# Kernel tuning notes

Hardware: AMD Instinct MI355X
Metric: run time of the kernel (lower is better)

The kernel has to match this reference:

```python
import jax, jax.numpy as jnp
import numpy as np

B, C, N, K, COUT = 8, 128, 10000, 16, 256


def setup_inputs() -> dict:
    key = jax.random.key(0)
    ks = jax.random.split(key, 8)
    x = jax.random.normal(ks[0], (B, C, N, 1), dtype=jnp.float32)
    edge_index = jax.random.randint(ks[1], (2, B, N, K), 0, N)
    s1 = 1.0 / np.sqrt(C)
    W1 = jax.random.uniform(ks[2], (C, C), jnp.float32, -s1, s1)   # nn1 1x1 conv weight
    b1 = jax.random.uniform(ks[3], (C,), jnp.float32, -s1, s1)
    Wp = jax.random.uniform(ks[4], (C, C), jnp.float32, -s1, s1)   # nn_pooling Linear
    bp = jax.random.uniform(ks[5], (C,), jnp.float32, -s1, s1)
    s2 = 1.0 / np.sqrt(2 * C)
    W2 = jax.random.uniform(ks[6], (COUT, 2 * C), jnp.float32, -s2, s2)  # nn2 1x1 conv
    b2 = jax.random.uniform(ks[7], (COUT,), jnp.float32, -s2, s2)
    return dict(x=x, edge_index=edge_index, W1=W1, b1=b1, Wp=Wp, bp=bp, W2=W2, b2=b2)


def reference(x, edge_index, W1, b1, Wp, bp, W2, b2):
    b, c, n, _ = x.shape
    k = edge_index.shape[-1]
    # nn1: 1x1 conv (channel mix) + ReLU -> [B,C,N,1]
    h = jax.nn.relu(jnp.einsum('bcns,dc->bdns', x, W1) + b1[None, :, None, None])
    # batched_index_select: gather neighbor features along vertex dim -> [B,C,N,K]
    hn = h[:, :, :, 0]                              # [B,C,N]
    idx = edge_index[0].reshape(b, 1, n * k)        # broadcast over C
    xj = jnp.take_along_axis(hn, idx, axis=2).reshape(b, c, n, k)
    # nn_pooling: Linear over channel dim + ReLU (transpose(1,3) in torch == act on C)
    xj = jax.nn.relu(jnp.einsum('bcnk,dc->bdnk', xj, Wp) + bp[None, :, None, None])
    # max-pool over neighbors, keepdim -> [B,C,N,1]
    xj = jnp.max(xj, axis=-1, keepdims=True)
    # concat along channels, nn2: 1x1 conv + ReLU -> [B,COUT,N,1]
    cat = jnp.concatenate([h, xj], axis=1)
    out = jax.nn.relu(jnp.einsum('bcns,dc->bdns', cat, W2) + b2[None, :, None, None])
    return out
```

## Files before the change

### kernel.cpp

```cpp
#include <hip/hip_runtime.h>

#define NODES 10000
#define BATCH 8
#define CH    128
#define KNB   16
#define CO    256

typedef __bf16 bf16x8 __attribute__((ext_vector_type(8)));
typedef float  f32x4  __attribute__((ext_vector_type(4)));

__device__ __forceinline__ unsigned short f2bf(float f) {
  unsigned u = __float_as_uint(f);
  u = (u + 0x7FFFu + ((u >> 16) & 1u)) >> 16;
  return (unsigned short)u;
}

__device__ __forceinline__ unsigned pkmax(unsigned a, unsigned b) {
  unsigned d;
  asm("v_pk_max_u16 %0, %1, %2" : "=v"(d) : "v"(a), "v"(b));
  return d;
}

__device__ __forceinline__ bf16x8 asbf8(uint4 u) {
  union { uint4 u; bf16x8 b; } c; c.u = u; return c.b;
}

__global__ __launch_bounds__(256) void prep(
    const float* __restrict__ W1, const float* __restrict__ Wp,
    const float* __restrict__ W2,
    unsigned short* __restrict__ W1b, unsigned short* __restrict__ Wpb,
    unsigned short* __restrict__ W2b)
{
  int i = blockIdx.x * 256 + threadIdx.x;
  const float* src; unsigned short* dst; int off;
  if (i < 4096)      { src = W1; dst = W1b; off = i; }
  else if (i < 8192) { src = Wp; dst = Wpb; off = i - 4096; }
  else               { src = W2; dst = W2b; off = i - 8192; }
  float4 v = ((const float4*)src)[off];
  ushort4 o;
  o.x = f2bf(v.x); o.y = f2bf(v.y); o.z = f2bf(v.z); o.w = f2bf(v.w);
  ((ushort4*)dst)[off] = o;
}

template<int MODE>
__global__ __launch_bounds__(256) void gemm_node(
    const unsigned short* __restrict__ Wb, const float* __restrict__ bias,
    const void* __restrict__ In, unsigned short* __restrict__ Out)
{
  const int b  = blockIdx.y;
  const int n0 = blockIdx.x * 64;
  const int t  = threadIdx.x;
  const int lane = t & 63, w = t >> 6;
  const int lm = lane & 15, q = lane >> 4;

  __shared__ unsigned short Bt[64 * 128];
  char* BtB = (char*)Bt;

  if (MODE == 0) {
    const float* X = (const float*)In + (size_t)b * CH * NODES;
#pragma unroll
    for (int rep = 0; rep < 4; ++rep) {
      int flat = t + rep * 256;
      int c2 = flat >> 4, n4 = flat & 15;
      int c  = c2 * 2;
      int gn = n0 + n4 * 4;
      float4 a0 = make_float4(0.f,0.f,0.f,0.f), a1 = a0;
      if (gn < NODES) {
        a0 = *(const float4*)(X + (size_t)c * NODES + gn);
        a1 = *(const float4*)(X + (size_t)(c + 1) * NODES + gn);
      }
      float v0[4] = {a0.x, a0.y, a0.z, a0.w};
      float v1[4] = {a1.x, a1.y, a1.z, a1.w};
#pragma unroll
      for (int i = 0; i < 4; ++i) {
        int nn = n4 * 4 + i;
        unsigned pk = (unsigned)f2bf(v0[i]) | ((unsigned)f2bf(v1[i]) << 16);
        int phys = nn * 256 + (((c2 >> 2) ^ (nn & 7)) << 4) + ((c2 & 3) << 2);
        *(unsigned*)(BtB + phys) = pk;
      }
    }
  } else {
    const unsigned short* H = (const unsigned short*)In + (size_t)b * NODES * CH;
#pragma unroll
    for (int rep = 0; rep < 4; ++rep) {
      int flat = t + rep * 256;
      int nl = flat >> 4, k16 = flat & 15;
      int gn = n0 + nl;
      uint4 v = make_uint4(0u,0u,0u,0u);
      if (gn < NODES) v = *(const uint4*)(H + (size_t)gn * CH + k16 * 8);
      int phys = nl * 256 + ((k16 ^ (nl & 7)) << 4);
      *(uint4*)(BtB + phys) = v;
    }
  }

  const int d0  = (w & 1) * 64;
  const int nbw = (w >> 1) * 32;

  uint4 af[4][4];
#pragma unroll
  for (int dt = 0; dt < 4; ++dt)
#pragma unroll
    for (int kt = 0; kt < 4; ++kt)
      af[dt][kt] = *(const uint4*)(Wb + (d0 + dt * 16 + lm) * CH + kt * 32 + q * 8);

  __syncthreads();

  f32x4 acc[4][2];
#pragma unroll
  for (int dt = 0; dt < 4; ++dt)
#pragma unroll
    for (int nt = 0; nt < 2; ++nt) acc[dt][nt] = (f32x4){0.f,0.f,0.f,0.f};

#pragma unroll
  for (int kt = 0; kt < 4; ++kt) {
#pragma unroll
    for (int nt = 0; nt < 2; ++nt) {
      int nl = nbw + nt * 16 + lm;
      int chunk = kt * 4 + q;
      int phys = nl * 256 + ((chunk ^ (nl & 7)) << 4);
      bf16x8 bb = asbf8(*(const uint4*)(BtB + phys));
#pragma unroll
      for (int dt = 0; dt < 4; ++dt)
        acc[dt][nt] = __builtin_amdgcn_mfma_f32_16x16x32_bf16(
            asbf8(af[dt][kt]), bb, acc[dt][nt], 0, 0, 0);
    }
  }

#pragma unroll
  for (int dt = 0; dt < 4; ++dt) {
    int dbase = d0 + dt * 16 + q * 4;
    float4 bi = *(const float4*)(bias + dbase);
    float bv[4] = {bi.x, bi.y, bi.z, bi.w};
#pragma unroll
    for (int nt = 0; nt < 2; ++nt) {
      int gn = n0 + nbw + nt * 16 + lm;
      if (gn < NODES) {
        ushort4 o;
        o.x = f2bf(fmaxf(acc[dt][nt][0] + bv[0], 0.f));
        o.y = f2bf(fmaxf(acc[dt][nt][1] + bv[1], 0.f));
        o.z = f2bf(fmaxf(acc[dt][nt][2] + bv[2], 0.f));
        o.w = f2bf(fmaxf(acc[dt][nt][3] + bv[3], 0.f));
        *(ushort4*)(Out + ((size_t)b * NODES + gn) * CH + dbase) = o;
      }
    }
  }
}

__global__ __launch_bounds__(256) void out_kernel(
    const unsigned short* __restrict__ h_t, const unsigned short* __restrict__ z_t,
    const int* __restrict__ e0, const unsigned short* __restrict__ W2b,
    const float* __restrict__ b2, float* __restrict__ out)
{
  const int bid = blockIdx.x;
  const int b   = bid & 7;
  const int n0  = (bid >> 3) * 64;
  const int t   = threadIdx.x;
  const int lane = t & 63, w = t >> 6;
  const int lm = lane & 15, q = lane >> 4;

  __shared__ unsigned short cat[64 * 256];
  char* catB = (char*)cat;

  {
    const unsigned short* H = h_t + (size_t)b * NODES * CH;
#pragma unroll
    for (int rep = 0; rep < 4; ++rep) {
      int flat = t + rep * 256;
      int nl = flat >> 4, k16 = flat & 15;
      int gn = n0 + nl;
      uint4 v = make_uint4(0u,0u,0u,0u);
      if (gn < NODES) v = *(const uint4*)(H + (size_t)gn * CH + k16 * 8);
      int phys = nl * 512 + ((k16 ^ (nl & 7)) << 4);
      *(uint4*)(catB + phys) = v;
    }
  }

  {
    const int nl = t & 63, cg = t >> 6;
    int gn = n0 + nl; if (gn > NODES - 1) gn = NODES - 1;
    const int* ep = e0 + ((size_t)b * NODES + gn) * KNB;
    const char* Z = (const char*)z_t + (size_t)b * NODES * CH * 2 + cg * 64;
    uint4 m0 = make_uint4(0u,0u,0u,0u), m1 = m0, m2 = m0, m3 = m0;
#pragma unroll
    for (int jq = 0; jq < 4; ++jq) {
      uint4 iv = *(const uint4*)(ep + jq * 4);
      unsigned idx4[4] = {iv.x, iv.y, iv.z, iv.w};
#pragma unroll
      for (int jj = 0; jj < 4; ++jj) {
        const uint4* p = (const uint4*)(Z + (size_t)idx4[jj] * (CH * 2));
        uint4 v0 = p[0], v1 = p[1], v2 = p[2], v3 = p[3];
        m0.x = pkmax(m0.x, v0.x); m0.y = pkmax(m0.y, v0.y);
        m0.z = pkmax(m0.z, v0.z); m0.w = pkmax(m0.w, v0.w);
        m1.x = pkmax(m1.x, v1.x); m1.y = pkmax(m1.y, v1.y);
        m1.z = pkmax(m1.z, v1.z); m1.w = pkmax(m1.w, v1.w);
        m2.x = pkmax(m2.x, v2.x); m2.y = pkmax(m2.y, v2.y);
        m2.z = pkmax(m2.z, v2.z); m2.w = pkmax(m2.w, v2.w);
        m3.x = pkmax(m3.x, v3.x); m3.y = pkmax(m3.y, v3.y);
        m3.z = pkmax(m3.z, v3.z); m3.w = pkmax(m3.w, v3.w);
      }
    }
    uint4 mm[4] = {m0, m1, m2, m3};
#pragma unroll
    for (int j = 0; j < 4; ++j) {
      int chunk = 16 + cg * 4 + j;
      int phys = nl * 512 + ((chunk ^ (nl & 7)) << 4);
      *(uint4*)(catB + phys) = mm[j];
    }
  }

  __syncthreads();

  const int d0 = w * 64;
  f32x4 acc[4][4];
#pragma unroll
  for (int dt = 0; dt < 4; ++dt)
#pragma unroll
    for (int nt = 0; nt < 4; ++nt) acc[dt][nt] = (f32x4){0.f,0.f,0.f,0.f};

  uint4 acur[4], anxt[4];
#pragma unroll
  for (int dt = 0; dt < 4; ++dt)
    acur[dt] = *(const uint4*)(W2b + (d0 + dt * 16 + lm) * CO + q * 8);

#pragma unroll
  for (int kt = 0; kt < 8; ++kt) {
    if (kt < 7) {
#pragma unroll
      for (int dt = 0; dt < 4; ++dt)
        anxt[dt] = *(const uint4*)(W2b + (d0 + dt * 16 + lm) * CO
                                   + (kt + 1) * 32 + q * 8);
    }
#pragma unroll
    for (int nt = 0; nt < 4; ++nt) {
      int nl = nt * 16 + lm;
      int chunk = kt * 4 + q;
      int phys = nl * 512 + ((chunk ^ (nl & 7)) << 4);
      bf16x8 bb = asbf8(*(const uint4*)(catB + phys));
#pragma unroll
      for (int dt = 0; dt < 4; ++dt)
        acc[dt][nt] = __builtin_amdgcn_mfma_f32_16x16x32_bf16(
            asbf8(acur[dt]), bb, acc[dt][nt], 0, 0, 0);
    }
#pragma unroll
    for (int dt = 0; dt < 4; ++dt) acur[dt] = anxt[dt];
  }

#pragma unroll
  for (int dt = 0; dt < 4; ++dt) {
    int dbase = d0 + dt * 16 + q * 4;
    float4 bi = *(const float4*)(b2 + dbase);
    float bv[4] = {bi.x, bi.y, bi.z, bi.w};
#pragma unroll
    for (int nt = 0; nt < 4; ++nt) {
      int gn = n0 + nt * 16 + lm;
      if (gn < NODES) {
        float* op = out + ((size_t)(b * CO + dbase) * NODES) + gn;
#pragma unroll
        for (int r = 0; r < 4; ++r)
          op[(size_t)r * NODES] = fmaxf(acc[dt][nt][r] + bv[r], 0.f);
      }
    }
  }
}

extern "C" void kernel_launch(void* const* d_in, const int* in_sizes, int n_in,
                              void* d_out, int out_size, void* d_ws, size_t ws_size,
                              hipStream_t stream) {
  const float* x  = (const float*)d_in[0];
  const int*   ei = (const int*)d_in[1];
  const float* W1 = (const float*)d_in[2];
  const float* b1 = (const float*)d_in[3];
  const float* Wp = (const float*)d_in[4];
  const float* bp = (const float*)d_in[5];
  const float* W2 = (const float*)d_in[6];
  const float* b2 = (const float*)d_in[7];
  float* out = (float*)d_out;

  unsigned short* ws  = (unsigned short*)d_ws;
  unsigned short* h_t = ws;
  unsigned short* z_t = h_t + (size_t)BATCH * NODES * CH;
  unsigned short* W1b = z_t + (size_t)BATCH * NODES * CH;
  unsigned short* Wpb = W1b + CH * CH;
  unsigned short* W2b = Wpb + CH * CH;

  prep<<<96, 256, 0, stream>>>(W1, Wp, W2, W1b, Wpb, W2b);

  dim3 g((NODES + 63) / 64, BATCH);
  gemm_node<0><<<g, 256, 0, stream>>>(W1b, b1, x, h_t);
  gemm_node<1><<<g, 256, 0, stream>>>(Wpb, bp, h_t, z_t);

  out_kernel<<<8 * ((NODES + 63) / 64), 256, 0, stream>>>(
      h_t, z_t, ei, W2b, b2, out);
}
```

Baseline: 229.7 us.

## Fuse nn1 and pooling GEMMs into one kernel; restructure neighbor gather

Merges the two per-node GEMM kernels into a single kernel that keeps the ReLU'd h tile in shared memory and feeds it straight into the Wp GEMM. This removes one launch and the global re-read of h. In out_kernel, neighbor indices are staged in shared memory first. The gather is remapped so four adjacent threads share a node and read contiguous 16-byte pieces of each neighbor row, which should improve coalescing. The cost is more LDS per block and an extra barrier.

After: 203.9 us. 1.13x faster.

```diff
diff --git a/kernel.cpp b/kernel.cpp
--- a/kernel.cpp
+++ b/kernel.cpp
@@ -20,7 +20,11 @@
   asm("v_pk_max_u16 %0, %1, %2" : "=v"(d) : "v"(a), "v"(b));
   return d;
 }
-
+__device__ __forceinline__ uint4 pkmax4(uint4 a, uint4 b) {
+  a.x = pkmax(a.x, b.x); a.y = pkmax(a.y, b.y);
+  a.z = pkmax(a.z, b.z); a.w = pkmax(a.w, b.w);
+  return a;
+}
 __device__ __forceinline__ bf16x8 asbf8(uint4 u) {
   union { uint4 u; bf16x8 b; } c; c.u = u; return c.b;
 }
@@ -42,10 +46,11 @@
   ((ushort4*)dst)[off] = o;
 }
 
-template<int MODE>
-__global__ __launch_bounds__(256) void gemm_node(
-    const unsigned short* __restrict__ Wb, const float* __restrict__ bias,
-    const void* __restrict__ In, unsigned short* __restrict__ Out)
+__global__ __launch_bounds__(256) void fused_hz(
+    const unsigned short* __restrict__ W1b, const float* __restrict__ b1,
+    const unsigned short* __restrict__ Wpb, const float* __restrict__ bp,
+    const float* __restrict__ x,
+    unsigned short* __restrict__ h_t, unsigned short* __restrict__ z_t)
 {
   const int b  = blockIdx.y;
   const int n0 = blockIdx.x * 64;
@@ -53,11 +58,13 @@
   const int lane = t & 63, w = t >> 6;
   const int lm = lane & 15, q = lane >> 4;
 
-  __shared__ unsigned short Bt[64 * 128];
+  __shared__ __align__(16) unsigned short Bt[64 * 128];
+  __shared__ __align__(16) unsigned short Ht[64 * 128];
   char* BtB = (char*)Bt;
-
-  if (MODE == 0) {
-    const float* X = (const float*)In + (size_t)b * CH * NODES;
+  char* HtB = (char*)Ht;
+
+  {
+    const float* X = x + (size_t)b * CH * NODES;
 #pragma unroll
     for (int rep = 0; rep < 4; ++rep) {
       int flat = t + rep * 256;
@@ -79,18 +86,6 @@
         *(unsigned*)(BtB + phys) = pk;
       }
     }
-  } else {
-    const unsigned short* H = (const unsigned short*)In + (size_t)b * NODES * CH;
-#pragma unroll
-    for (int rep = 0; rep < 4; ++rep) {
-      int flat = t + rep * 256;
-      int nl = flat >> 4, k16 = flat & 15;
-      int gn = n0 + nl;
-      uint4 v = make_uint4(0u,0u,0u,0u);
-      if (gn < NODES) v = *(const uint4*)(H + (size_t)gn * CH + k16 * 8);
-      int phys = nl * 256 + ((k16 ^ (nl & 7)) << 4);
-      *(uint4*)(BtB + phys) = v;
-    }
   }
 
   const int d0  = (w & 1) * 64;
@@ -101,7 +96,7 @@
   for (int dt = 0; dt < 4; ++dt)
 #pragma unroll
     for (int kt = 0; kt < 4; ++kt)
-      af[dt][kt] = *(const uint4*)(Wb + (d0 + dt * 16 + lm) * CH + kt * 32 + q * 8);
+      af[dt][kt] = *(const uint4*)(W1b + (d0 + dt*16 + lm) * CH + kt*32 + q*8);
 
   __syncthreads();
 
@@ -112,7 +107,7 @@
     for (int nt = 0; nt < 2; ++nt) acc[dt][nt] = (f32x4){0.f,0.f,0.f,0.f};
 
 #pragma unroll
-  for (int kt = 0; kt < 4; ++kt) {
+  for (int kt = 0; kt < 4; ++kt)
 #pragma unroll
     for (int nt = 0; nt < 2; ++nt) {
       int nl = nbw + nt * 16 + lm;
@@ -124,12 +119,61 @@
         acc[dt][nt] = __builtin_amdgcn_mfma_f32_16x16x32_bf16(
             asbf8(af[dt][kt]), bb, acc[dt][nt], 0, 0, 0);
     }
-  }
+
+  uint4 af2[4][4];
+#pragma unroll
+  for (int dt = 0; dt < 4; ++dt)
+#pragma unroll
+    for (int kt = 0; kt < 4; ++kt)
+      af2[dt][kt] = *(const uint4*)(Wpb + (d0 + dt*16 + lm) * CH + kt*32 + q*8);
 
 #pragma unroll
   for (int dt = 0; dt < 4; ++dt) {
     int dbase = d0 + dt * 16 + q * 4;
-    float4 bi = *(const float4*)(bias + dbase);
+    float4 bi = *(const float4*)(b1 + dbase);
+    float bv[4] = {bi.x, bi.y, bi.z, bi.w};
+#pragma unroll
+    for (int nt = 0; nt < 2; ++nt) {
+      int nl = nbw + nt * 16 + lm;
+      int gn = n0 + nl;
+      ushort4 o;
+      o.x = f2bf(fmaxf(acc[dt][nt][0] + bv[0], 0.f));
+      o.y = f2bf(fmaxf(acc[dt][nt][1] + bv[1], 0.f));
+      o.z = f2bf(fmaxf(acc[dt][nt][2] + bv[2], 0.f));
+      o.w = f2bf(fmaxf(acc[dt][nt][3] + bv[3], 0.f));
+      int chunk = dbase >> 3;
+      int phys  = nl * 256 + ((chunk ^ (nl & 7)) << 4) + ((q & 1) << 3);
+      *(ushort4*)(HtB + phys) = o;
+      if (gn < NODES)
+        *(ushort4*)(h_t + ((size_t)b * NODES + gn) * CH + dbase) = o;
+    }
+  }
+
+  __syncthreads();
+
+#pragma unroll
+  for (int dt = 0; dt < 4; ++dt)
+#pragma unroll
+    for (int nt = 0; nt < 2; ++nt) acc[dt][nt] = (f32x4){0.f,0.f,0.f,0.f};
+
+#pragma unroll
+  for (int kt = 0; kt < 4; ++kt)
+#pragma unroll
+    for (int nt = 0; nt < 2; ++nt) {
+      int nl = nbw + nt * 16 + lm;
+      int chunk = kt * 4 + q;
+      int phys = nl * 256 + ((chunk ^ (nl & 7)) << 4);
+      bf16x8 bb = asbf8(*(const uint4*)(HtB + phys));
+#pragma unroll
+      for (int dt = 0; dt < 4; ++dt)
+        acc[dt][nt] = __builtin_amdgcn_mfma_f32_16x16x32_bf16(
+            asbf8(af2[dt][kt]), bb, acc[dt][nt], 0, 0, 0);
+    }
+
+#pragma unroll
+  for (int dt = 0; dt < 4; ++dt) {
+    int dbase = d0 + dt * 16 + q * 4;
+    float4 bi = *(const float4*)(bp + dbase);
     float bv[4] = {bi.x, bi.y, bi.z, bi.w};
 #pragma unroll
     for (int nt = 0; nt < 2; ++nt) {
@@ -140,7 +184,7 @@
         o.y = f2bf(fmaxf(acc[dt][nt][1] + bv[1], 0.f));
         o.z = f2bf(fmaxf(acc[dt][nt][2] + bv[2], 0.f));
         o.w = f2bf(fmaxf(acc[dt][nt][3] + bv[3], 0.f));
-        *(ushort4*)(Out + ((size_t)b * NODES + gn) * CH + dbase) = o;
+        *(ushort4*)(z_t + ((size_t)b * NODES + gn) * CH + dbase) = o;
       }
     }
   }
@@ -158,8 +202,39 @@
   const int lane = t & 63, w = t >> 6;
   const int lm = lane & 15, q = lane >> 4;
 
-  __shared__ unsigned short cat[64 * 256];
+  __shared__ __align__(16) unsigned short cat[64 * 256];
+  __shared__ __align__(16) int idxs[64 * KNB];
   char* catB = (char*)cat;
+
+  {
+    int nl = t >> 2, jq = t & 3;
+    int gn = n0 + nl; if (gn > NODES - 1) gn = NODES - 1;
+    uint4 iv = *(const uint4*)(e0 + ((size_t)b * NODES + gn) * KNB + jq * 4);
+    *(uint4*)&idxs[nl * KNB + jq * 4] = iv;
+  }
+  __syncthreads();
+
+  {
+    const int nl = t >> 2, c = t & 3;
+    const char* Z = (const char*)z_t + (size_t)b * NODES * CH * 2 + c * 16;
+    uint4 m[4];
+#pragma unroll
+    for (int cg = 0; cg < 4; ++cg) m[cg] = make_uint4(0u, 0u, 0u, 0u);
+#pragma unroll
+    for (int k = 0; k < KNB; ++k) {
+      int jn = idxs[nl * KNB + k];
+      const char* p = Z + (size_t)jn * (CH * 2);
+#pragma unroll
+      for (int cg = 0; cg < 4; ++cg)
+        m[cg] = pkmax4(m[cg], *(const uint4*)(p + cg * 64));
+    }
+#pragma unroll
+    for (int cg = 0; cg < 4; ++cg) {
+      int chunk = 16 + cg * 4 + c;
+      int phys = nl * 512 + ((chunk ^ (nl & 7)) << 4);
+      *(uint4*)(catB + phys) = m[cg];
+    }
+  }
 
   {
     const unsigned short* H = h_t + (size_t)b * NODES * CH;
@@ -168,46 +243,13 @@
       int flat = t + rep * 256;
       int nl = flat >> 4, k16 = flat & 15;
       int gn = n0 + nl;
-      uint4 v = make_uint4(0u,0u,0u,0u);
+      uint4 v = make_uint4(0u, 0u, 0u, 0u);
       if (gn < NODES) v = *(const uint4*)(H + (size_t)gn * CH + k16 * 8);
       int phys = nl * 512 + ((k16 ^ (nl & 7)) << 4);
       *(uint4*)(catB + phys) = v;
     }
   }
 
-  {
-    const int nl = t & 63, cg = t >> 6;
-    int gn = n0 + nl; if (gn > NODES - 1) gn = NODES - 1;
-    const int* ep = e0 + ((size_t)b * NODES + gn) * KNB;
-    const char* Z = (const char*)z_t + (size_t)b * NODES * CH * 2 + cg * 64;
-    uint4 m0 = make_uint4(0u,0u,0u,0u), m1 = m0, m2 = m0, m3 = m0;
-#pragma unroll
-    for (int jq = 0; jq < 4; ++jq) {
-      uint4 iv = *(const uint4*)(ep + jq * 4);
-      unsigned idx4[4] = {iv.x, iv.y, iv.z, iv.w};
-#pragma unroll
-      for (int jj = 0; jj < 4; ++jj) {
-        const uint4* p = (const uint4*)(Z + (size_t)idx4[jj] * (CH * 2));
-        uint4 v0 = p[0], v1 = p[1], v2 = p[2], v3 = p[3];
-        m0.x = pkmax(m0.x, v0.x); m0.y = pkmax(m0.y, v0.y);
-        m0.z = pkmax(m0.z, v0.z); m0.w = pkmax(m0.w, v0.w);
-        m1.x = pkmax(m1.x, v1.x); m1.y = pkmax(m1.y, v1.y);
-        m1.z = pkmax(m1.z, v1.z); m1.w = pkmax(m1.w, v1.w);
-        m2.x = pkmax(m2.x, v2.x); m2.y = pkmax(m2.y, v2.y);
-        m2.z = pkmax(m2.z, v2.z); m2.w = pkmax(m2.w, v2.w);
-        m3.x = pkmax(m3.x, v3.x); m3.y = pkmax(m3.y, v3.y);
-        m3.z = pkmax(m3.z, v3.z); m3.w = pkmax(m3.w, v3.w);
-      }
-    }
-    uint4 mm[4] = {m0, m1, m2, m3};
-#pragma unroll
-    for (int j = 0; j < 4; ++j) {
-      int chunk = 16 + cg * 4 + j;
-      int phys = nl * 512 + ((chunk ^ (nl & 7)) << 4);
-      *(uint4*)(catB + phys) = mm[j];
-    }
-  }
-
   __syncthreads();
 
   const int d0 = w * 64;
@@ -215,7 +257,7 @@
 #pragma unroll
   for (int dt = 0; dt < 4; ++dt)
 #pragma unroll
-    for (int nt = 0; nt < 4; ++nt) acc[dt][nt] = (f32x4){0.f,0.f,0.f,0.f};
+    for (int nt = 0; nt < 4; ++nt) acc[dt][nt] = (f32x4){0.f, 0.f, 0.f, 0.f};
 
   uint4 acur[4], anxt[4];
 #pragma unroll
@@ -285,10 +327,7 @@
 
   prep<<<96, 256, 0, stream>>>(W1, Wp, W2, W1b, Wpb, W2b);
 
-  dim3 g((NODES + 63) / 64, BATCH);
-  gemm_node<0><<<g, 256, 0, stream>>>(W1b, b1, x, h_t);
-  gemm_node<1><<<g, 256, 0, stream>>>(Wpb, bp, h_t, z_t);
-
-  out_kernel<<<8 * ((NODES + 63) / 64), 256, 0, stream>>>(
-      h_t, z_t, ei, W2b, b2, out);
-}
+  const int NT = (NODES + 63) / 64;
+  fused_hz<<<dim3(NT, BATCH), 256, 0, stream>>>(W1b, b1, Wpb, bp, x, h_t, z_t);
+  out_kernel<<<BATCH * NT, 256, 0, stream>>>(h_t, z_t, ei, W2b, b2, out);
+}
```

## Fuse nn1 and pooling GEMMs into one kernel, restructure output kernel per-wave

Applied to the files above, without the earlier changes.

Merges the two node GEMM kernels into one fused_hz kernel. Each wave computes h for 16 nodes, stages them in its own LDS slice, and immediately applies the pooling-linear GEMM, so h is not re-read from global memory between launches. The output kernel shrinks to 128-thread blocks where each wave independently gathers h and neighbor max for 32 nodes. It then runs the W2 GEMM from register-held B fragments without a block-wide barrier. The trade-off is that weights are streamed from global/L1 per wave instead of being shared across waves, and the x loads become strided per-lane reads.

Measured after the change: 230.9 us. About the same (+0.5%).

```diff
diff --git a/kernel.cpp b/kernel.cpp
--- a/kernel.cpp
+++ b/kernel.cpp
@@ -14,13 +14,19 @@
   u = (u + 0x7FFFu + ((u >> 16) & 1u)) >> 16;
   return (unsigned short)u;
 }
-
+__device__ __forceinline__ unsigned pk2(float a, float b) {
+  return (unsigned)f2bf(a) | ((unsigned)f2bf(b) << 16);
+}
 __device__ __forceinline__ unsigned pkmax(unsigned a, unsigned b) {
   unsigned d;
   asm("v_pk_max_u16 %0, %1, %2" : "=v"(d) : "v"(a), "v"(b));
   return d;
 }
-
+__device__ __forceinline__ uint4 pkmax4(uint4 a, uint4 b) {
+  a.x = pkmax(a.x, b.x); a.y = pkmax(a.y, b.y);
+  a.z = pkmax(a.z, b.z); a.w = pkmax(a.w, b.w);
+  return a;
+}
 __device__ __forceinline__ bf16x8 asbf8(uint4 u) {
   union { uint4 u; bf16x8 b; } c; c.u = u; return c.b;
 }
@@ -42,224 +48,224 @@
   ((ushort4*)dst)[off] = o;
 }
 
-template<int MODE>
-__global__ __launch_bounds__(256) void gemm_node(
-    const unsigned short* __restrict__ Wb, const float* __restrict__ bias,
-    const void* __restrict__ In, unsigned short* __restrict__ Out)
+__global__ __launch_bounds__(256) void fused_hz(
+    const unsigned short* __restrict__ W1b, const float* __restrict__ b1,
+    const unsigned short* __restrict__ Wpb, const float* __restrict__ bp,
+    const float* __restrict__ x,
+    unsigned short* __restrict__ h_t, unsigned short* __restrict__ z_t)
 {
-  const int b  = blockIdx.y;
-  const int n0 = blockIdx.x * 64;
-  const int t  = threadIdx.x;
-  const int lane = t & 63, w = t >> 6;
-  const int lm = lane & 15, q = lane >> 4;
-
-  __shared__ unsigned short Bt[64 * 128];
-  char* BtB = (char*)Bt;
-
-  if (MODE == 0) {
-    const float* X = (const float*)In + (size_t)b * CH * NODES;
-#pragma unroll
-    for (int rep = 0; rep < 4; ++rep) {
-      int flat = t + rep * 256;
-      int c2 = flat >> 4, n4 = flat & 15;
-      int c  = c2 * 2;
-      int gn = n0 + n4 * 4;
-      float4 a0 = make_float4(0.f,0.f,0.f,0.f), a1 = a0;
-      if (gn < NODES) {
-        a0 = *(const float4*)(X + (size_t)c * NODES + gn);
-        a1 = *(const float4*)(X + (size_t)(c + 1) * NODES + gn);
-      }
-      float v0[4] = {a0.x, a0.y, a0.z, a0.w};
-      float v1[4] = {a1.x, a1.y, a1.z, a1.w};
-#pragma unroll
-      for (int i = 0; i < 4; ++i) {
-        int nn = n4 * 4 + i;
-        unsigned pk = (unsigned)f2bf(v0[i]) | ((unsigned)f2bf(v1[i]) << 16);
-        int phys = nn * 256 + (((c2 >> 2) ^ (nn & 7)) << 4) + ((c2 & 3) << 2);
-        *(unsigned*)(BtB + phys) = pk;
-      }
-    }
-  } else {
-    const unsigned short* H = (const unsigned short*)In + (size_t)b * NODES * CH;
-#pragma unroll
-    for (int rep = 0; rep < 4; ++rep) {
-      int flat = t + rep * 256;
-      int nl = flat >> 4, k16 = flat & 15;
-      int gn = n0 + nl;
-      uint4 v = make_uint4(0u,0u,0u,0u);
-      if (gn < NODES) v = *(const uint4*)(H + (size_t)gn * CH + k16 * 8);
-      int phys = nl * 256 + ((k16 ^ (nl & 7)) << 4);
-      *(uint4*)(BtB + phys) = v;
-    }
-  }
-
-  const int d0  = (w & 1) * 64;
-  const int nbw = (w >> 1) * 32;
-
-  uint4 af[4][4];
-#pragma unroll
-  for (int dt = 0; dt < 4; ++dt)
+  const int b    = blockIdx.y;
+  const int t    = threadIdx.x;
+  const int w    = t >> 6, lane = t & 63;
+  const int lm   = lane & 15, q = lane >> 4;
+  const int nw0  = blockIdx.x * 64 + w * 16;
+
+  __shared__ __align__(16) unsigned short Hs_all[4][16 * 128];
+  char* Hs = (char*)Hs_all[w];
+
+  const int node = nw0 + lm;
+  const int gn   = (node < NODES) ? node : (NODES - 1);
+
+  const float* X = x + (size_t)b * CH * NODES + gn;
+  float xv[4][8];
+#pragma unroll
+  for (int kt = 0; kt < 4; ++kt)
+#pragma unroll
+    for (int j = 0; j < 8; ++j)
+      xv[kt][j] = X[(size_t)(kt * 32 + q * 8 + j) * NODES];
+
+  uint4 B1[4];
+#pragma unroll
+  for (int kt = 0; kt < 4; ++kt) {
+    B1[kt].x = pk2(xv[kt][0], xv[kt][1]);
+    B1[kt].y = pk2(xv[kt][2], xv[kt][3]);
+    B1[kt].z = pk2(xv[kt][4], xv[kt][5]);
+    B1[kt].w = pk2(xv[kt][6], xv[kt][7]);
+  }
+
+  uint4 a_cur[4], a_nxt[4];
+#pragma unroll
+  for (int kt = 0; kt < 4; ++kt)
+    a_cur[kt] = *(const uint4*)(W1b + (size_t)(lm) * CH + kt * 32 + q * 8);
+
+#pragma unroll
+  for (int dt = 0; dt < 8; ++dt) {
+    if (dt < 7) {
+#pragma unroll
+      for (int kt = 0; kt < 4; ++kt)
+        a_nxt[kt] = *(const uint4*)(W1b + (size_t)((dt + 1) * 16 + lm) * CH
+                                    + kt * 32 + q * 8);
+    }
+    f32x4 acc = (f32x4){0.f, 0.f, 0.f, 0.f};
 #pragma unroll
     for (int kt = 0; kt < 4; ++kt)
-      af[dt][kt] = *(const uint4*)(Wb + (d0 + dt * 16 + lm) * CH + kt * 32 + q * 8);
-
-  __syncthreads();
-
-  f32x4 acc[4][2];
-#pragma unroll
-  for (int dt = 0; dt < 4; ++dt)
-#pragma unroll
-    for (int nt = 0; nt < 2; ++nt) acc[dt][nt] = (f32x4){0.f,0.f,0.f,0.f};
-
-#pragma unroll
-  for (int kt = 0; kt < 4; ++kt) {
-#pragma unroll
-    for (int nt = 0; nt < 2; ++nt) {
-      int nl = nbw + nt * 16 + lm;
-      int chunk = kt * 4 + q;
-      int phys = nl * 256 + ((chunk ^ (nl & 7)) << 4);
-      bf16x8 bb = asbf8(*(const uint4*)(BtB + phys));
-#pragma unroll
-      for (int dt = 0; dt < 4; ++dt)
-        acc[dt][nt] = __builtin_amdgcn_mfma_f32_16x16x32_bf16(
-            asbf8(af[dt][kt]), bb, acc[dt][nt], 0, 0, 0);
-    }
-  }
-
-#pragma unroll
-  for (int dt = 0; dt < 4; ++dt) {
-    int dbase = d0 + dt * 16 + q * 4;
-    float4 bi = *(const float4*)(bias + dbase);
-    float bv[4] = {bi.x, bi.y, bi.z, bi.w};
-#pragma unroll
-    for (int nt = 0; nt < 2; ++nt) {
-      int gn = n0 + nbw + nt * 16 + lm;
-      if (gn < NODES) {
-        ushort4 o;
-        o.x = f2bf(fmaxf(acc[dt][nt][0] + bv[0], 0.f));
-        o.y = f2bf(fmaxf(acc[dt][nt][1] + bv[1], 0.f));
-        o.z = f2bf(fmaxf(acc[dt][nt][2] + bv[2], 0.f));
-        o.w = f2bf(fmaxf(acc[dt][nt][3] + bv[3], 0.f));
-        *(ushort4*)(Out + ((size_t)b * NODES + gn) * CH + dbase) = o;
-      }
-    }
-  }
-}
-
-__global__ __launch_bounds__(256) void out_kernel(
+      acc = __builtin_amdgcn_mfma_f32_16x16x32_bf16(
+          asbf8(a_cur[kt]), asbf8(B1[kt]), acc, 0, 0, 0);
+
+    const int d0 = dt * 16 + q * 4;
+    float4 bi = *(const float4*)(b1 + d0);
+    ushort4 o;
+    o.x = f2bf(fmaxf(acc[0] + bi.x, 0.f));
+    o.y = f2bf(fmaxf(acc[1] + bi.y, 0.f));
+    o.z = f2bf(fmaxf(acc[2] + bi.z, 0.f));
+    o.w = f2bf(fmaxf(acc[3] + bi.w, 0.f));
+    if (node < NODES)
+      *(ushort4*)(h_t + ((size_t)b * NODES + node) * CH + d0) = o;
+    const int chunk = dt * 2 + (q >> 1);
+    *(ushort4*)(Hs + lm * 256 + ((chunk ^ (lm & 7)) << 4) + ((q & 1) << 3)) = o;
+#pragma unroll
+    for (int kt = 0; kt < 4; ++kt) a_cur[kt] = a_nxt[kt];
+  }
+
+  uint4 B2[4];
+#pragma unroll
+  for (int kt = 0; kt < 4; ++kt)
+    B2[kt] = *(const uint4*)(Hs + lm * 256 + (((kt * 4 + q) ^ (lm & 7)) << 4));
+
+#pragma unroll
+  for (int kt = 0; kt < 4; ++kt)
+    a_cur[kt] = *(const uint4*)(Wpb + (size_t)(lm) * CH + kt * 32 + q * 8);
+
+#pragma unroll
+  for (int dt = 0; dt < 8; ++dt) {
+    if (dt < 7) {
+#pragma unroll
+      for (int kt = 0; kt < 4; ++kt)
+        a_nxt[kt] = *(const uint4*)(Wpb + (size_t)((dt + 1) * 16 + lm) * CH
+                                    + kt * 32 + q * 8);
+    }
+    f32x4 acc = (f32x4){0.f, 0.f, 0.f, 0.f};
+#pragma unroll
+    for (int kt = 0; kt < 4; ++kt)
+      acc = __builtin_amdgcn_mfma_f32_16x16x32_bf16(
+          asbf8(a_cur[kt]), asbf8(B2[kt]), acc, 0, 0, 0);
+
+    const int d0 = dt * 16 + q * 4;
+    float4 bi = *(const float4*)(bp + d0);
+    if (node < NODES) {
+      ushort4 o;
+      o.x = f2bf(fmaxf(acc[0] + bi.x, 0.f));
+      o.y = f2bf(fmaxf(acc[1] + bi.y, 0.f));
+      o.z = f2bf(fmaxf(acc[2] + bi.z, 0.f));
+      o.w = f2bf(fmaxf(acc[3] + bi.w, 0.f));
+      *(ushort4*)(z_t + ((size_t)b * NODES + node) * CH + d0) = o;
+    }
+#pragma unroll
+    for (int kt = 0; kt < 4; ++kt) a_cur[kt] = a_nxt[kt];
+  }
+}
+
+__global__ __launch_bounds__(128) void out_kernel(
     const unsigned short* __restrict__ h_t, const unsigned short* __restrict__ z_t,
     const int* __restrict__ e0, const unsigned short* __restrict__ W2b,
     const float* __restrict__ b2, float* __restrict__ out)
 {
   const int bid = blockIdx.x;
   const int b   = bid & 7;
-  const int n0  = (bid >> 3) * 64;
   const int t   = threadIdx.x;
-  const int lane = t & 63, w = t >> 6;
-  const int lm = lane & 15, q = lane >> 4;
-
-  __shared__ unsigned short cat[64 * 256];
-  char* catB = (char*)cat;
-
-  {
-    const unsigned short* H = h_t + (size_t)b * NODES * CH;
-#pragma unroll
-    for (int rep = 0; rep < 4; ++rep) {
-      int flat = t + rep * 256;
-      int nl = flat >> 4, k16 = flat & 15;
-      int gn = n0 + nl;
-      uint4 v = make_uint4(0u,0u,0u,0u);
-      if (gn < NODES) v = *(const uint4*)(H + (size_t)gn * CH + k16 * 8);
-      int phys = nl * 512 + ((k16 ^ (nl & 7)) << 4);
-      *(uint4*)(catB + phys) = v;
-    }
-  }
-
-  {
-    const int nl = t & 63, cg = t >> 6;
-    int gn = n0 + nl; if (gn > NODES - 1) gn = NODES - 1;
+  const int w   = t >> 6, lane = t & 63;
+  const int nw0 = (bid >> 3) * 64 + w * 32;
+
+  __shared__ __align__(16) unsigned short cat_all[2][32 * 256];
+  char* cat = (char*)cat_all[w];
+
+  const int nl4 = lane >> 2, c = lane & 3;
+  const char* Zb = (const char*)z_t + (size_t)b * NODES * (CH * 2);
+#pragma unroll
+  for (int p = 0; p < 2; ++p) {
+    const int nl = p * 16 + nl4;
+    int gn = nw0 + nl; if (gn >= NODES) gn = NODES - 1;
+
+    const char* H = (const char*)h_t + ((size_t)b * NODES + gn) * (CH * 2);
+    uint4 hv[4];
+#pragma unroll
+    for (int j = 0; j < 4; ++j)
+      hv[j] = *(const uint4*)(H + ((4 * j + c) << 4));
+
     const int* ep = e0 + ((size_t)b * NODES + gn) * KNB;
-    const char* Z = (const char*)z_t + (size_t)b * NODES * CH * 2 + cg * 64;
-    uint4 m0 = make_uint4(0u,0u,0u,0u), m1 = m0, m2 = m0, m3 = m0;
+    unsigned idxv[KNB];
 #pragma unroll
     for (int jq = 0; jq < 4; ++jq) {
       uint4 iv = *(const uint4*)(ep + jq * 4);
-      unsigned idx4[4] = {iv.x, iv.y, iv.z, iv.w};
-#pragma unroll
-      for (int jj = 0; jj < 4; ++jj) {
-        const uint4* p = (const uint4*)(Z + (size_t)idx4[jj] * (CH * 2));
-        uint4 v0 = p[0], v1 = p[1], v2 = p[2], v3 = p[3];
-        m0.x = pkmax(m0.x, v0.x); m0.y = pkmax(m0.y, v0.y);
-        m0.z = pkmax(m0.z, v0.z); m0.w = pkmax(m0.w, v0.w);
-        m1.x = pkmax(m1.x, v1.x); m1.y = pkmax(m1.y, v1.y);
-        m1.z = pkmax(m1.z, v1.z); m1.w = pkmax(m1.w, v1.w);
-        m2.x = pkmax(m2.x, v2.x); m2.y = pkmax(m2.y, v2.y);
-        m2.z = pkmax(m2.z, v2.z); m2.w = pkmax(m2.w, v2.w);
-        m3.x = pkmax(m3.x, v3.x); m3.y = pkmax(m3.y, v3.y);
-        m3.z = pkmax(m3.z, v3.z); m3.w = pkmax(m3.w, v3.w);
+      idxv[jq * 4 + 0] = iv.x; idxv[jq * 4 + 1] = iv.y;
+      idxv[jq * 4 + 2] = iv.z; idxv[jq * 4 + 3] = iv.w;
+    }
+
+    uint4 m[4];
+#pragma unroll
+    for (int j = 0; j < 4; ++j) m[j] = make_uint4(0u, 0u, 0u, 0u);
+#pragma unroll
+    for (int k = 0; k < KNB; ++k) {
+      const char* pz = Zb + (size_t)idxv[k] * (CH * 2);
+#pragma unroll
+      for (int j = 0; j < 4; ++j)
+        m[j] = pkmax4(m[j], *(const uint4*)(pz + ((4 * j + c) << 4)));
+    }
+
+#pragma unroll
+    for (int j = 0; j < 4; ++j) {
+      const int ch = 4 * j + c;
+      *(uint4*)(cat + nl * 512 + ((ch ^ (nl & 7)) << 4)) = hv[j];
+      const int cz = 16 + 4 * j + c;
+      *(uint4*)(cat + nl * 512 + ((cz ^ (nl & 7)) << 4)) = m[j];
+    }
+  }
+
+  const int lm = lane & 15, q = lane >> 4;
+  uint4 Bf[2][8];
+#pragma unroll
+  for (int nt = 0; nt < 2; ++nt)
+#pragma unroll
+    for (int kt = 0; kt < 8; ++kt)
+      Bf[nt][kt] = *(const uint4*)(cat + (nt * 16 + lm) * 512
+                                   + (((kt * 4 + q) ^ (lm & 7)) << 4));
+
+  uint4 a_cur[4], a_nxt[4];
+#pragma unroll
+  for (int kt = 0; kt < 4; ++kt)
+    a_cur[kt] = *(const uint4*)(W2b + (size_t)lm * CO + kt * 32 + q * 8);
+
+  f32x4 acc0 = (f32x4){0.f, 0.f, 0.f, 0.f};
+  f32x4 acc1 = (f32x4){0.f, 0.f, 0.f, 0.f};
+
+#pragma unroll
+  for (int s = 0; s < 32; ++s) {
+    const int dt = s >> 1, half = s & 1;
+    if (s < 31) {
+      const int dn = (s + 1) >> 1, hn = (s + 1) & 1;
+#pragma unroll
+      for (int kt = 0; kt < 4; ++kt)
+        a_nxt[kt] = *(const uint4*)(W2b + (size_t)(dn * 16 + lm) * CO
+                                    + (hn * 4 + kt) * 32 + q * 8);
+    }
+#pragma unroll
+    for (int kt = 0; kt < 4; ++kt) {
+      const int ktg = half * 4 + kt;
+      acc0 = __builtin_amdgcn_mfma_f32_16x16x32_bf16(
+          asbf8(a_cur[kt]), asbf8(Bf[0][ktg]), acc0, 0, 0, 0);
+      acc1 = __builtin_amdgcn_mfma_f32_16x16x32_bf16(
+          asbf8(a_cur[kt]), asbf8(Bf[1][ktg]), acc1, 0, 0, 0);
+    }
+    if (half == 1) {
+      const int d0 = dt * 16 + q * 4;
+      float4 bi = *(const float4*)(b2 + d0);
+      float bv[4] = {bi.x, bi.y, bi.z, bi.w};
+      f32x4 aa[2] = {acc0, acc1};
+#pragma unroll
+      for (int nt = 0; nt < 2; ++nt) {
+        const int gn = nw0 + nt * 16 + lm;
+        if (gn < NODES) {
+          float* op = out + (size_t)(b * CO + d0) * NODES + gn;
+#pragma unroll
+          for (int r = 0; r < 4; ++r)
+            op[(size_t)r * NODES] = fmaxf(aa[nt][r] + bv[r], 0.f);
+        }
       }
-    }
-    uint4 mm[4] = {m0, m1, m2, m3};
-#pragma unroll
-    for (int j = 0; j < 4; ++j) {
-      int chunk = 16 + cg * 4 + j;
-      int phys = nl * 512 + ((chunk ^ (nl & 7)) << 4);
-      *(uint4*)(catB + phys) = mm[j];
-    }
-  }
-
-  __syncthreads();
-
-  const int d0 = w * 64;
-  f32x4 acc[4][4];
-#pragma unroll
-  for (int dt = 0; dt < 4; ++dt)
-#pragma unroll
-    for (int nt = 0; nt < 4; ++nt) acc[dt][nt] = (f32x4){0.f,0.f,0.f,0.f};
-
-  uint4 acur[4], anxt[4];
-#pragma unroll
-  for (int dt = 0; dt < 4; ++dt)
-    acur[dt] = *(const uint4*)(W2b + (d0 + dt * 16 + lm) * CO + q * 8);
-
-#pragma unroll
-  for (int kt = 0; kt < 8; ++kt) {
-    if (kt < 7) {
-#pragma unroll
-      for (int dt = 0; dt < 4; ++dt)
-        anxt[dt] = *(const uint4*)(W2b + (d0 + dt * 16 + lm) * CO
-                                   + (kt + 1) * 32 + q * 8);
-    }
-#pragma unroll
-    for (int nt = 0; nt < 4; ++nt) {
-      int nl = nt * 16 + lm;
-      int chunk = kt * 4 + q;
-      int phys = nl * 512 + ((chunk ^ (nl & 7)) << 4);
-      bf16x8 bb = asbf8(*(const uint4*)(catB + phys));
-#pragma unroll
-      for (int dt = 0; dt < 4; ++dt)
-        acc[dt][nt] = __builtin_amdgcn_mfma_f32_16x16x32_bf16(
-            asbf8(acur[dt]), bb, acc[dt][nt], 0, 0, 0);
-    }
-#pragma unroll
-    for (int dt = 0; dt < 4; ++dt) acur[dt] = anxt[dt];
-  }
-
-#pragma unroll
-  for (int dt = 0; dt < 4; ++dt) {
-    int dbase = d0 + dt * 16 + q * 4;
-    float4 bi = *(const float4*)(b2 + dbase);
-    float bv[4] = {bi.x, bi.y, bi.z, bi.w};
-#pragma unroll
-    for (int nt = 0; nt < 4; ++nt) {
-      int gn = n0 + nt * 16 + lm;
-      if (gn < NODES) {
-        float* op = out + ((size_t)(b * CO + dbase) * NODES) + gn;
-#pragma unroll
-        for (int r = 0; r < 4; ++r)
-          op[(size_t)r * NODES] = fmaxf(acc[dt][nt][r] + bv[r], 0.f);
-      }
-    }
+      acc0 = (f32x4){0.f, 0.f, 0.f, 0.f};
+      acc1 = (f32x4){0.f, 0.f, 0.f, 0.f};
+    }
+#pragma unroll
+    for (int kt = 0; kt < 4; ++kt) a_cur[kt] = a_nxt[kt];
   }
 }
 
@@ -285,10 +291,7 @@
 
   prep<<<96, 256, 0, stream>>>(W1, Wp, W2, W1b, Wpb, W2b);
 
-  dim3 g((NODES + 63) / 64, BATCH);
-  gemm_node<0><<<g, 256, 0, stream>>>(W1b, b1, x, h_t);
-  gemm_node<1><<<g, 256, 0, stream>>>(Wpb, bp, h_t, z_t);
-
-  out_kernel<<<8 * ((NODES + 63) / 64), 256, 0, stream>>>(
-      h_t, z_t, ei, W2b, b2, out);
-}
+  const int NT = (NODES + 63) / 64;
+  fused_hz<<<dim3(NT, BATCH), 256, 0, stream>>>(W1b, b1, Wpb, bp, x, h_t, z_t);
+  out_kernel<<<BATCH * NT, 128, 0, stream>>>(h_t, z_t, ei, W2b, b2, out);
+}
```
